# Kernel tuning notes

Hardware: AMD Instinct MI355X
Metric: run time of the kernel (lower is better)

The kernel has to match this reference:

```python
import jax, jax.numpy as jnp
import numpy as np

USER_NUM = 100000
ITEM_NUM = 50000
N_NODES = USER_NUM + ITEM_NUM
NNZ = 4800000
HIDE_DIM = 128
SLOPE = 0.2
EPS = 1e-12  # F.normalize eps


def setup_inputs() -> dict:
    key = jax.random.key(0)
    ks = jax.random.split(key, 9)
    rows = jax.random.randint(ks[0], (NNZ,), 0, N_NODES, dtype=jnp.int32)
    cols = jax.random.randint(ks[1], (NNZ,), 0, N_NODES, dtype=jnp.int32)
    vals = jax.random.uniform(ks[2], (NNZ,), dtype=jnp.float32)
    user_emb = jax.random.normal(ks[3], (USER_NUM, HIDE_DIM), dtype=jnp.float32) * 0.1
    item_emb = jax.random.normal(ks[4], (ITEM_NUM, HIDE_DIM), dtype=jnp.float32) * 0.1
    u_w0 = jax.random.normal(ks[5], (HIDE_DIM, HIDE_DIM), dtype=jnp.float32) * 0.05
    v_w0 = jax.random.normal(ks[6], (HIDE_DIM, HIDE_DIM), dtype=jnp.float32) * 0.05
    u_w1 = jax.random.normal(ks[7], (HIDE_DIM, HIDE_DIM), dtype=jnp.float32) * 0.05
    v_w1 = jax.random.normal(ks[8], (HIDE_DIM, HIDE_DIM), dtype=jnp.float32) * 0.05
    return {"rows": rows, "cols": cols, "vals": vals,
            "user_emb": user_emb, "item_emb": item_emb,
            "u_w0": u_w0, "v_w0": v_w0, "u_w1": u_w1, "v_w1": v_w1}


def _spmm(rows, cols, vals, feat):
    # sparse [N,N] @ dense [N,D] via gather + segment_sum
    gathered = vals[:, None] * feat[cols]            # [nnz, D]
    return jax.ops.segment_sum(gathered, rows, num_segments=N_NODES)


def _gcn_layer(rows, cols, vals, u_feat, i_feat, u_w, v_w):
    feat = jnp.concatenate([u_feat @ u_w, i_feat @ v_w], axis=0)  # [N, D]
    return jax.nn.leaky_relu(_spmm(rows, cols, vals, feat), negative_slope=SLOPE)


def _l2norm(x):
    n = jnp.sqrt(jnp.sum(x * x, axis=1, keepdims=True))
    return x / jnp.maximum(n, EPS)


def reference(rows, cols, vals, user_emb, item_emb, u_w0, v_w0, u_w1, v_w1):
    all_u = [user_emb]
    all_i = [item_emb]
    # layer 0 consumes raw embeddings
    emb = _gcn_layer(rows, cols, vals, user_emb, item_emb, u_w0, v_w0)
    norm = _l2norm(emb)
    all_u.append(norm[:USER_NUM]); all_i.append(norm[USER_NUM:])
    # layer 1 consumes UNNORMALIZED previous layer output (as in the torch code)
    emb = _gcn_layer(rows, cols, vals, emb[:USER_NUM], emb[USER_NUM:], u_w1, v_w1)
    norm = _l2norm(emb)
    all_u.append(norm[:USER_NUM]); all_i.append(norm[USER_NUM:])
    user_embedding = jnp.concatenate(all_u, axis=1)  # [userNum, 3*D]
    item_embedding = jnp.concatenate(all_i, axis=1)  # [itemNum, 3*D]
    return (user_embedding, item_embedding)
```

## Files before the change

### kernel.cpp

```cpp
#include <hip/hip_runtime.h>

#define D 128
#define OUTD 384
#define SLOPE 0.2f
#define BSH 7
#define BROWS 128
#define MAXNB 2048
#define FCAP 4736
#define SPAN 8192
#define SCT 512

typedef __attribute__((ext_vector_type(8))) short bf16x8;
typedef __attribute__((ext_vector_type(4))) float f32x4;

__device__ __forceinline__ unsigned f2bf(float f) {
    unsigned u = __float_as_uint(f);
    return (u + 0x7FFFu + ((u >> 16) & 1u)) >> 16;
}

__device__ __forceinline__ void nt_store_f4(float4 v, float* p) {
    f32x4 t = {v.x, v.y, v.z, v.w};
    __builtin_nontemporal_store(t, (f32x4*)p);
}

__global__ __launch_bounds__(256) void wt_prep(const float* __restrict__ W0,
                                               const float* __restrict__ W1,
                                               const float* __restrict__ W2,
                                               const float* __restrict__ W3,
                                               unsigned short* __restrict__ wt) {
    const float* Ws[4] = {W0, W1, W2, W3};
    const float* W = Ws[blockIdx.x];
    unsigned short* o = wt + (size_t)blockIdx.x * 16384;
    for (int i = threadIdx.x; i < 16384; i += 256) {
        int k = i >> 7, n = i & 127;
        o[(size_t)n * 128 + k] = (unsigned short)f2bf(W[(size_t)k * 128 + n]);
    }
}

#define GR 64
#define APAD 136
__global__ __launch_bounds__(256) void gemm_mfma(const float* __restrict__ in, int pitch,
                                                 const unsigned short* __restrict__ Wt,
                                                 unsigned short* __restrict__ featb,
                                                 const float* __restrict__ rowscale,
                                                 float* __restrict__ rawout,
                                                 int nrows) {
    __shared__ unsigned short sA[GR * APAD];
    __shared__ unsigned short sW[128 * APAD];
    int tid = threadIdx.x;
    int row0 = blockIdx.x * GR;
    int nr = min(GR, nrows - row0);

    for (int i = tid; i < GR * 32; i += 256) {
        int r = i >> 5, c4 = (i & 31) * 4;
        unsigned lo = 0, hi = 0;
        if (r < nr) {
            float4 t = *(const float4*)&in[(size_t)(row0 + r) * pitch + c4];
            if (rawout)
                nt_store_f4(t, &rawout[(size_t)(row0 + r) * OUTD + c4]);
            if (rowscale) {
                float s = rowscale[row0 + r];
                t.x *= s; t.y *= s; t.z *= s; t.w *= s;
            }
            lo = f2bf(t.x) | (f2bf(t.y) << 16);
            hi = f2bf(t.z) | (f2bf(t.w) << 16);
        }
        uint2 pk = {lo, hi};
        *(uint2*)&sA[r * APAD + c4] = pk;
    }
    for (int i = tid; i < 128 * 16; i += 256) {
        int n = i >> 4, k8 = (i & 15) * 8;
        *(uint4*)&sW[n * APAD + k8] = *(const uint4*)&Wt[(size_t)n * 128 + k8];
    }
    __syncthreads();

    int l  = tid & 63;
    int w  = tid >> 6;
    int lr = l & 15;
    int lk = (l >> 4) * 8;

    f32x4 acc[8];
#pragma unroll
    for (int t = 0; t < 8; ++t) acc[t] = (f32x4){0.f, 0.f, 0.f, 0.f};

#pragma unroll
    for (int k0 = 0; k0 < 128; k0 += 32) {
        bf16x8 af = *(const bf16x8*)&sA[(16 * w + lr) * APAD + k0 + lk];
#pragma unroll
        for (int t = 0; t < 8; ++t) {
            bf16x8 bf = *(const bf16x8*)&sW[(t * 16 + lr) * APAD + k0 + lk];
            acc[t] = __builtin_amdgcn_mfma_f32_16x16x32_bf16(af, bf, acc[t], 0, 0, 0);
        }
    }

    int rbase = 16 * w + (l >> 4) * 4;
#pragma unroll
    for (int t = 0; t < 8; ++t) {
#pragma unroll
        for (int q = 0; q < 4; ++q) {
            int r = rbase + q;
            if (r < nr)
                featb[(size_t)(row0 + r) * D + t * 16 + lr] = (unsigned short)f2bf(acc[t][q]);
        }
    }
}


__global__ __launch_bounds__(256) void init_cursors(int* __restrict__ bcursor,
                                                    int NB, int cap) {
    int b = blockIdx.x * 256 + threadIdx.x;
    if (b < NB) bcursor[b * 16] = b * cap;
}

#define EMIT(r, c, v)                                                              \
    {                                                                              \
        int b_ = (r) >> BSH;                                                       \
        int pos_ = atomicAdd(&hist[b_], 1);                                        \
        if ((unsigned)(pos_ - b_ * cap) < (unsigned)cap)                           \
            etmp[pos_] = make_uint2(((unsigned)((r) & (BROWS - 1)) << 18) |        \
                                    (unsigned)(c), __float_as_uint(v));            \
    }

__global__ __launch_bounds__(SCT) void chunk_scatter(const int* __restrict__ rows,
                                                     const int* __restrict__ cols,
                                                     const float* __restrict__ vals,
                                                     int* __restrict__ bcursor,
                                                     uint2* __restrict__ etmp,
                                                     int nnz, int NB, int cap) {
    __shared__ int hist[MAXNB];
    int tid = threadIdx.x;
    int lo  = blockIdx.x * SPAN;
    int hi  = min(lo + SPAN, nnz);
    if (lo >= nnz) return;

    for (int i = tid; i < NB; i += SCT) hist[i] = 0;
    __syncthreads();

    int4 r4[4];
#pragma unroll
    for (int q = 0; q < 4; ++q) {
        int e = lo + (q * SCT + tid) * 4;
        if (e + 3 < hi) {
            r4[q] = *(const int4*)&rows[e];
            atomicAdd(&hist[r4[q].x >> BSH], 1);
            atomicAdd(&hist[r4[q].y >> BSH], 1);
            atomicAdd(&hist[r4[q].z >> BSH], 1);
            atomicAdd(&hist[r4[q].w >> BSH], 1);
        } else {
            int t0 = (e + 0 < hi) ? rows[e + 0] : -1;
            int t1 = (e + 1 < hi) ? rows[e + 1] : -1;
            int t2 = (e + 2 < hi) ? rows[e + 2] : -1;
            int t3 = (e + 3 < hi) ? rows[e + 3] : -1;
            if (t0 >= 0) atomicAdd(&hist[t0 >> BSH], 1);
            if (t1 >= 0) atomicAdd(&hist[t1 >> BSH], 1);
            if (t2 >= 0) atomicAdd(&hist[t2 >> BSH], 1);
            if (t3 >= 0) atomicAdd(&hist[t3 >> BSH], 1);
            r4[q] = make_int4(t0, t1, t2, t3);
        }
    }
    __syncthreads();

    for (int i = tid; i < NB; i += SCT) {
        int c = hist[i];
        hist[i] = c ? atomicAdd(&bcursor[i * 16], c) : 0;
    }
    __syncthreads();

#pragma unroll
    for (int q = 0; q < 4; ++q) {
        int e = lo + (q * SCT + tid) * 4;
        if (e + 3 < hi) {
            int4   c4 = *(const int4*)&cols[e];
            float4 v4 = *(const float4*)&vals[e];
            EMIT(r4[q].x, c4.x, v4.x);
            EMIT(r4[q].y, c4.y, v4.y);
            EMIT(r4[q].z, c4.z, v4.z);
            EMIT(r4[q].w, c4.w, v4.w);
        } else {
            int rr0 = r4[q].x, rr1 = r4[q].y, rr2 = r4[q].z, rr3 = r4[q].w;
            if (rr0 >= 0) { EMIT(rr0, cols[e + 0], vals[e + 0]); }
            if (rr1 >= 0) { EMIT(rr1, cols[e + 1], vals[e + 1]); }
            if (rr2 >= 0) { EMIT(rr2, cols[e + 2], vals[e + 2]); }
            if (rr3 >= 0) { EMIT(rr3, cols[e + 3], vals[e + 3]); }
        }
    }
}

#define FTH 512
__global__ __launch_bounds__(FTH) void bucket_finalize(const int* __restrict__ bcursor,
                                                       uint2* __restrict__ ep,
                                                       int* __restrict__ row_start,
                                                       int* __restrict__ rend,
                                                       int N, int cap) {
    __shared__ uint2 ed[FCAP];
    __shared__ int rcnt[BROWS], rbase[BROWS];
    __shared__ int wsum[2];
    int b   = blockIdx.x;
    int s   = b * cap;
    int len = bcursor[b * 16] - s;
    if (len > cap) len = cap;
    int tid = threadIdx.x;
    if (tid < BROWS) rcnt[tid] = 0;
    __syncthreads();

    for (int i = tid; i < len; i += FTH) {
        uint2 t = ep[s + i];
        ed[i] = t;
        atomicAdd(&rcnt[t.x >> 18], 1);
    }
    __syncthreads();

    int lane = tid & 63, wid = tid >> 6;
    int c = (tid < BROWS) ? rcnt[tid] : 0;
    int incl = c;
#pragma unroll
    for (int off = 1; off < 64; off <<= 1) {
        int t = __shfl_up(incl, off);
        if (lane >= off) incl += t;
    }
    if (tid < BROWS && lane == 63) wsum[wid] = incl;
    __syncthreads();
    if (tid < BROWS) {
        int woff = (wid == 1) ? wsum[0] : 0;
        int excl = woff + incl - c;
        rbase[tid] = s + excl;
        int row = b * BROWS + tid;
        if (row < N) { row_start[row] = s + excl; rend[row] = s + excl + c; }
    }
    __syncthreads();

    for (int i = tid; i < len; i += FTH) {
        uint2 t = ed[i];
        int rl = t.x >> 18;
        int pos = atomicAdd(&rbase[rl], 1);
        ep[pos] = make_uint2(t.x & 0x3FFFFu, t.y);
    }
}

#define ACCQ(vbits, g)                                             \
    {                                                              \
        float v = __uint_as_float(vbits);                          \
        acc0.x += v * __uint_as_float((g).x << 16);                \
        acc0.y += v * __uint_as_float((g).x & 0xFFFF0000u);        \
        acc0.z += v * __uint_as_float((g).y << 16);                \
        acc0.w += v * __uint_as_float((g).y & 0xFFFF0000u);        \
        acc1.x += v * __uint_as_float((g).z << 16);                \
        acc1.y += v * __uint_as_float((g).z & 0xFFFF0000u);        \
        acc1.z += v * __uint_as_float((g).w << 16);                \
        acc1.w += v * __uint_as_float((g).w & 0xFFFF0000u);        \
    }

__global__ __launch_bounds__(256) void spmm_csr4(const uint2* __restrict__ ep,
                                                 const int* __restrict__ rstart,
                                                 const int* __restrict__ rend,
                                                 const unsigned short* __restrict__ featb,
                                                 float* __restrict__ out,
                                                 float* __restrict__ nsave,
                                                 int col_off, int N) {
    int row  = blockIdx.x * 4 + (threadIdx.x >> 6);
    if (row >= N) return;
    int lane = threadIdx.x & 63;
    int j = lane & 15;
    int h = lane >> 4;
    int s = rstart[row], e = rend[row];

    float4 acc0 = {0.f, 0.f, 0.f, 0.f};
    float4 acc1 = {0.f, 0.f, 0.f, 0.f};
    int i = s;
    for (; i + 16 <= e; i += 16) {
        uint2 eA = ep[i + h];
        uint2 eB = ep[i + 4 + h];
        uint2 eC = ep[i + 8 + h];
        uint2 eD = ep[i + 12 + h];
        uint4 gA = *(const uint4*)&featb[(size_t)eA.x * D + j * 8];
        uint4 gB = *(const uint4*)&featb[(size_t)eB.x * D + j * 8];
        uint4 gC = *(const uint4*)&featb[(size_t)eC.x * D + j * 8];
        uint4 gD = *(const uint4*)&featb[(size_t)eD.x * D + j * 8];
        ACCQ(eA.y, gA);
        ACCQ(eB.y, gB);
        ACCQ(eC.y, gC);
        ACCQ(eD.y, gD);
    }
    for (; i + 8 <= e; i += 8) {
        uint2 eA = ep[i + h];
        uint2 eB = ep[i + 4 + h];
        uint4 gA = *(const uint4*)&featb[(size_t)eA.x * D + j * 8];
        uint4 gB = *(const uint4*)&featb[(size_t)eB.x * D + j * 8];
        ACCQ(eA.y, gA);
        ACCQ(eB.y, gB);
    }
    for (; i < e; i += 4) {
        int idx = i + h;
        uint2 ev = make_uint2(0u, 0u);
        if (idx < e) ev = ep[idx];
        uint4 g = *(const uint4*)&featb[(size_t)ev.x * D + j * 8];
        ACCQ(ev.y, g);
    }

#pragma unroll
    for (int m = 16; m <= 32; m <<= 1) {
        acc0.x += __shfl_xor(acc0.x, m);
        acc0.y += __shfl_xor(acc0.y, m);
        acc0.z += __shfl_xor(acc0.z, m);
        acc0.w += __shfl_xor(acc0.w, m);
        acc1.x += __shfl_xor(acc1.x, m);
        acc1.y += __shfl_xor(acc1.y, m);
        acc1.z += __shfl_xor(acc1.z, m);
        acc1.w += __shfl_xor(acc1.w, m);
    }

    acc0.x = (acc0.x > 0.f) ? acc0.x : SLOPE * acc0.x;
    acc0.y = (acc0.y > 0.f) ? acc0.y : SLOPE * acc0.y;
    acc0.z = (acc0.z > 0.f) ? acc0.z : SLOPE * acc0.z;
    acc0.w = (acc0.w > 0.f) ? acc0.w : SLOPE * acc0.w;
    acc1.x = (acc1.x > 0.f) ? acc1.x : SLOPE * acc1.x;
    acc1.y = (acc1.y > 0.f) ? acc1.y : SLOPE * acc1.y;
    acc1.z = (acc1.z > 0.f) ? acc1.z : SLOPE * acc1.z;
    acc1.w = (acc1.w > 0.f) ? acc1.w : SLOPE * acc1.w;

    float ss = acc0.x * acc0.x + acc0.y * acc0.y + acc0.z * acc0.z + acc0.w * acc0.w
             + acc1.x * acc1.x + acc1.y * acc1.y + acc1.z * acc1.z + acc1.w * acc1.w;
#pragma unroll
    for (int m = 8; m >= 1; m >>= 1) ss += __shfl_xor(ss, m);
    float nm = fmaxf(sqrtf(ss), 1e-12f);
    float sc = 1.0f / nm;

    if (nsave && lane == 0) nsave[row] = nm;
    if (h == 0) {
        float* dst = &out[(size_t)row * OUTD + col_off + j * 8];
        float4 o0 = {acc0.x * sc, acc0.y * sc, acc0.z * sc, acc0.w * sc};
        float4 o1 = {acc1.x * sc, acc1.y * sc, acc1.z * sc, acc1.w * sc};
        *(float4*)&dst[0] = o0;
        *(float4*)&dst[4] = o1;
    }
}

extern "C" void kernel_launch(void* const* d_in, const int* in_sizes, int n_in,
                              void* d_out, int out_size, void* d_ws, size_t ws_size,
                              hipStream_t stream) {
    const int*   rows = (const int*)d_in[0];
    const int*   cols = (const int*)d_in[1];
    const float* vals = (const float*)d_in[2];
    const float* ue   = (const float*)d_in[3];
    const float* ie   = (const float*)d_in[4];
    const float* uw0  = (const float*)d_in[5];
    const float* vw0  = (const float*)d_in[6];
    const float* uw1  = (const float*)d_in[7];
    const float* vw1  = (const float*)d_in[8];
    float* out = (float*)d_out;

    int nnz = in_sizes[0];
    int U   = in_sizes[3] / D;
    int I   = in_sizes[4] / D;
    int N   = U + I;
    int NB  = (N + BROWS - 1) >> BSH;

    int avg = nnz / NB;
    int cap = avg + avg / 8 + 64;
    if (cap > FCAP) cap = FCAP;

    char* p = (char*)d_ws;
    unsigned short* featb = (unsigned short*)p;  p += (size_t)N * D * 2;
    uint2* edges          = (uint2*)p;           p += (size_t)NB * cap * 8;
    int* row_start        = (int*)p;             p += (size_t)N * 4;
    int* rend             = (int*)p;             p += (size_t)N * 4;
    float* nsave          = (float*)p;           p += (size_t)N * 4;
    p = (char*)(((size_t)p + 63) & ~(size_t)63);
    int* bcursor          = (int*)p;             p += (size_t)NB * 64;
    unsigned short* wtbuf = (unsigned short*)p;  p += (size_t)4 * 16384 * 2;

    int row_blocks = (N + 3) / 4;
    int gu = (U + GR - 1) / GR;
    int gi = (I + GR - 1) / GR;
    int sc_blocks = (nnz + SPAN - 1) / SPAN;

    wt_prep<<<4, 256, 0, stream>>>(uw0, vw0, uw1, vw1, wtbuf);
    init_cursors<<<(NB + 255) / 256, 256, 0, stream>>>(bcursor, NB, cap);

    chunk_scatter<<<sc_blocks, SCT, 0, stream>>>(rows, cols, vals, bcursor, edges,
                                                 nnz, NB, cap);
    bucket_finalize<<<NB, FTH, 0, stream>>>(bcursor, edges, row_start, rend, N, cap);

    gemm_mfma<<<gu, 256, 0, stream>>>(ue, D, wtbuf, featb, nullptr, out, U);
    gemm_mfma<<<gi, 256, 0, stream>>>(ie, D, wtbuf + 16384, featb + (size_t)U * D,
                                      nullptr, out + (size_t)U * OUTD, I);
    spmm_csr4<<<row_blocks, 256, 0, stream>>>(edges, row_start, rend, featb, out,
                                              nsave, D, N);

    gemm_mfma<<<gu, 256, 0, stream>>>(out + D, OUTD, wtbuf + 2 * 16384, featb,
                                      nsave, nullptr, U);
    gemm_mfma<<<gi, 256, 0, stream>>>(out + (size_t)U * OUTD + D, OUTD, wtbuf + 3 * 16384,
                                      featb + (size_t)U * D, nsave + U, nullptr, I);
    spmm_csr4<<<row_blocks, 256, 0, stream>>>(edges, row_start, rend, featb, out,
                                              nullptr, 2 * D, N);
}
```

Measured before the change: 628.7 us.

## Fuse per-bucket edge sort with first-layer SpMM into one kernel

Merges bucket_finalize and the first spmm_csr4 launch into one kernel. Each 512-thread block sorts its 128-row bucket and then computes SpMM, leaky-ReLU and L2 normalisation for those rows, with each wave handling 16 rows. This removes one launch and lets the just-written sorted edges be read back while likely still cached. In exchange it cuts parallelism to one block per 128 rows, and the large LDS footprint may limit occupancy during the gather phase.

```diff
diff --git a/kernel.cpp b/kernel.cpp
--- a/kernel.cpp
+++ b/kernel.cpp
@@ -104,7 +104,6 @@
         }
     }
 }
-
 
 __global__ __launch_bounds__(256) void init_cursors(int* __restrict__ bcursor,
                                                     int NB, int cap) {
@@ -186,57 +185,6 @@
     }
 }
 
-#define FTH 512
-__global__ __launch_bounds__(FTH) void bucket_finalize(const int* __restrict__ bcursor,
-                                                       uint2* __restrict__ ep,
-                                                       int* __restrict__ row_start,
-                                                       int* __restrict__ rend,
-                                                       int N, int cap) {
-    __shared__ uint2 ed[FCAP];
-    __shared__ int rcnt[BROWS], rbase[BROWS];
-    __shared__ int wsum[2];
-    int b   = blockIdx.x;
-    int s   = b * cap;
-    int len = bcursor[b * 16] - s;
-    if (len > cap) len = cap;
-    int tid = threadIdx.x;
-    if (tid < BROWS) rcnt[tid] = 0;
-    __syncthreads();
-
-    for (int i = tid; i < len; i += FTH) {
-        uint2 t = ep[s + i];
-        ed[i] = t;
-        atomicAdd(&rcnt[t.x >> 18], 1);
-    }
-    __syncthreads();
-
-    int lane = tid & 63, wid = tid >> 6;
-    int c = (tid < BROWS) ? rcnt[tid] : 0;
-    int incl = c;
-#pragma unroll
-    for (int off = 1; off < 64; off <<= 1) {
-        int t = __shfl_up(incl, off);
-        if (lane >= off) incl += t;
-    }
-    if (tid < BROWS && lane == 63) wsum[wid] = incl;
-    __syncthreads();
-    if (tid < BROWS) {
-        int woff = (wid == 1) ? wsum[0] : 0;
-        int excl = woff + incl - c;
-        rbase[tid] = s + excl;
-        int row = b * BROWS + tid;
-        if (row < N) { row_start[row] = s + excl; rend[row] = s + excl + c; }
-    }
-    __syncthreads();
-
-    for (int i = tid; i < len; i += FTH) {
-        uint2 t = ed[i];
-        int rl = t.x >> 18;
-        int pos = atomicAdd(&rbase[rl], 1);
-        ep[pos] = make_uint2(t.x & 0x3FFFFu, t.y);
-    }
-}
-
 #define ACCQ(vbits, g)                                             \
     {                                                              \
         float v = __uint_as_float(vbits);                          \
@@ -250,12 +198,146 @@
         acc1.w += v * __uint_as_float((g).w & 0xFFFF0000u);        \
     }
 
+#define FTH 512
+__global__ __launch_bounds__(FTH) void spmm_sort_fused(const int* __restrict__ bcursor,
+                                                       uint2* __restrict__ ep,
+                                                       int* __restrict__ row_start,
+                                                       int* __restrict__ rend,
+                                                       const unsigned short* __restrict__ featb,
+                                                       float* __restrict__ out,
+                                                       float* __restrict__ nsave,
+                                                       int col_off, int N, int cap) {
+    __shared__ uint2 ed[FCAP];
+    __shared__ int rcnt[BROWS], rbase[BROWS], rsLds[BROWS];
+    __shared__ int wsum[2];
+    int b   = blockIdx.x;
+    int s   = b * cap;
+    int len = bcursor[b * 16] - s;
+    if (len > cap) len = cap;
+    int tid = threadIdx.x;
+    if (tid < BROWS) rcnt[tid] = 0;
+    __syncthreads();
+
+    for (int i = tid; i < len; i += FTH) {
+        uint2 t = ep[s + i];
+        ed[i] = t;
+        atomicAdd(&rcnt[t.x >> 18], 1);
+    }
+    __syncthreads();
+
+    int lane = tid & 63, wid = tid >> 6;
+    int c = (tid < BROWS) ? rcnt[tid] : 0;
+    int incl = c;
+#pragma unroll
+    for (int off = 1; off < 64; off <<= 1) {
+        int t = __shfl_up(incl, off);
+        if (lane >= off) incl += t;
+    }
+    if (tid < BROWS && lane == 63) wsum[wid] = incl;
+    __syncthreads();
+    if (tid < BROWS) {
+        int woff = (wid == 1) ? wsum[0] : 0;
+        int excl = woff + incl - c;
+        rbase[tid] = s + excl;
+        rsLds[tid] = s + excl;
+        int row = b * BROWS + tid;
+        if (row < N) { row_start[row] = s + excl; rend[row] = s + excl + c; }
+    }
+    __syncthreads();
+
+    for (int i = tid; i < len; i += FTH) {
+        uint2 t = ed[i];
+        int pos = atomicAdd(&rbase[t.x >> 18], 1);
+        ep[pos] = make_uint2(t.x & 0x3FFFFu, t.y);
+    }
+    __syncthreads();
+
+    int j = lane & 15;
+    int h = lane >> 4;
+    for (int rr = 0; rr < 16; ++rr) {
+        int rloc = wid * 16 + rr;
+        int row  = b * BROWS + rloc;
+        if (row >= N) break;
+        int sE = rsLds[rloc];
+        int eE = sE + rcnt[rloc];
+
+        float4 acc0 = {0.f, 0.f, 0.f, 0.f};
+        float4 acc1 = {0.f, 0.f, 0.f, 0.f};
+        int i = sE;
+        for (; i + 16 <= eE; i += 16) {
+            uint2 eA = ep[i + h];
+            uint2 eB = ep[i + 4 + h];
+            uint2 eC = ep[i + 8 + h];
+            uint2 eD = ep[i + 12 + h];
+            uint4 gA = *(const uint4*)&featb[(size_t)eA.x * D + j * 8];
+            uint4 gB = *(const uint4*)&featb[(size_t)eB.x * D + j * 8];
+            uint4 gC = *(const uint4*)&featb[(size_t)eC.x * D + j * 8];
+            uint4 gD = *(const uint4*)&featb[(size_t)eD.x * D + j * 8];
+            ACCQ(eA.y, gA);
+            ACCQ(eB.y, gB);
+            ACCQ(eC.y, gC);
+            ACCQ(eD.y, gD);
+        }
+        for (; i + 8 <= eE; i += 8) {
+            uint2 eA = ep[i + h];
+            uint2 eB = ep[i + 4 + h];
+            uint4 gA = *(const uint4*)&featb[(size_t)eA.x * D + j * 8];
+            uint4 gB = *(const uint4*)&featb[(size_t)eB.x * D + j * 8];
+            ACCQ(eA.y, gA);
+            ACCQ(eB.y, gB);
+        }
+        for (; i < eE; i += 4) {
+            int idx = i + h;
+            uint2 ev = make_uint2(0u, 0u);
+            if (idx < eE) ev = ep[idx];
+            uint4 g = *(const uint4*)&featb[(size_t)ev.x * D + j * 8];
+            ACCQ(ev.y, g);
+        }
+
+#pragma unroll
+        for (int m = 16; m <= 32; m <<= 1) {
+            acc0.x += __shfl_xor(acc0.x, m);
+            acc0.y += __shfl_xor(acc0.y, m);
+            acc0.z += __shfl_xor(acc0.z, m);
+            acc0.w += __shfl_xor(acc0.w, m);
+            acc1.x += __shfl_xor(acc1.x, m);
+            acc1.y += __shfl_xor(acc1.y, m);
+            acc1.z += __shfl_xor(acc1.z, m);
+            acc1.w += __shfl_xor(acc1.w, m);
+        }
+
+        acc0.x = (acc0.x > 0.f) ? acc0.x : SLOPE * acc0.x;
+        acc0.y = (acc0.y > 0.f) ? acc0.y : SLOPE * acc0.y;
+        acc0.z = (acc0.z > 0.f) ? acc0.z : SLOPE * acc0.z;
+        acc0.w = (acc0.w > 0.f) ? acc0.w : SLOPE * acc0.w;
+        acc1.x = (acc1.x > 0.f) ? acc1.x : SLOPE * acc1.x;
+        acc1.y = (acc1.y > 0.f) ? acc1.y : SLOPE * acc1.y;
+        acc1.z = (acc1.z > 0.f) ? acc1.z : SLOPE * acc1.z;
+        acc1.w = (acc1.w > 0.f) ? acc1.w : SLOPE * acc1.w;
+
+        float ss = acc0.x * acc0.x + acc0.y * acc0.y + acc0.z * acc0.z + acc0.w * acc0.w
+                 + acc1.x * acc1.x + acc1.y * acc1.y + acc1.z * acc1.z + acc1.w * acc1.w;
+#pragma unroll
+        for (int m = 8; m >= 1; m >>= 1) ss += __shfl_xor(ss, m);
+        float nm = fmaxf(sqrtf(ss), 1e-12f);
+        float sc = 1.0f / nm;
+
+        if (lane == 0) nsave[row] = nm;
+        if (h == 0) {
+            float* dst = &out[(size_t)row * OUTD + col_off + j * 8];
+            float4 o0 = {acc0.x * sc, acc0.y * sc, acc0.z * sc, acc0.w * sc};
+            float4 o1 = {acc1.x * sc, acc1.y * sc, acc1.z * sc, acc1.w * sc};
+            *(float4*)&dst[0] = o0;
+            *(float4*)&dst[4] = o1;
+        }
+    }
+}
+
 __global__ __launch_bounds__(256) void spmm_csr4(const uint2* __restrict__ ep,
                                                  const int* __restrict__ rstart,
                                                  const int* __restrict__ rend,
                                                  const unsigned short* __restrict__ featb,
                                                  float* __restrict__ out,
-                                                 float* __restrict__ nsave,
                                                  int col_off, int N) {
     int row  = blockIdx.x * 4 + (threadIdx.x >> 6);
     if (row >= N) return;
@@ -322,10 +404,8 @@
              + acc1.x * acc1.x + acc1.y * acc1.y + acc1.z * acc1.z + acc1.w * acc1.w;
 #pragma unroll
     for (int m = 8; m >= 1; m >>= 1) ss += __shfl_xor(ss, m);
-    float nm = fmaxf(sqrtf(ss), 1e-12f);
-    float sc = 1.0f / nm;
-
-    if (nsave && lane == 0) nsave[row] = nm;
+    float sc = 1.0f / fmaxf(sqrtf(ss), 1e-12f);
+
     if (h == 0) {
         float* dst = &out[(size_t)row * OUTD + col_off + j * 8];
         float4 o0 = {acc0.x * sc, acc0.y * sc, acc0.z * sc, acc0.w * sc};
@@ -379,18 +459,18 @@
 
     chunk_scatter<<<sc_blocks, SCT, 0, stream>>>(rows, cols, vals, bcursor, edges,
                                                  nnz, NB, cap);
-    bucket_finalize<<<NB, FTH, 0, stream>>>(bcursor, edges, row_start, rend, N, cap);
 
     gemm_mfma<<<gu, 256, 0, stream>>>(ue, D, wtbuf, featb, nullptr, out, U);
     gemm_mfma<<<gi, 256, 0, stream>>>(ie, D, wtbuf + 16384, featb + (size_t)U * D,
                                       nullptr, out + (size_t)U * OUTD, I);
-    spmm_csr4<<<row_blocks, 256, 0, stream>>>(edges, row_start, rend, featb, out,
-                                              nsave, D, N);
+
+    spmm_sort_fused<<<NB, FTH, 0, stream>>>(bcursor, edges, row_start, rend, featb,
+                                            out, nsave, D, N, cap);
 
     gemm_mfma<<<gu, 256, 0, stream>>>(out + D, OUTD, wtbuf + 2 * 16384, featb,
                                       nsave, nullptr, U);
     gemm_mfma<<<gi, 256, 0, stream>>>(out + (size_t)U * OUTD + D, OUTD, wtbuf + 3 * 16384,
                                       featb + (size_t)U * D, nsave + U, nullptr, I);
     spmm_csr4<<<row_blocks, 256, 0, stream>>>(edges, row_start, rend, featb, out,
-                                              nullptr, 2 * D, N);
-}
+                                              2 * D, N);
+}
```

Result: slower. 648.4 us (+3.1%).

## Replace global-atomic bucket scatter with per-segment local sort plus offset matrix

Applied to the files above, without the earlier changes.

The COO-to-CSR build no longer uses global atomic cursors per bucket. Each segment now sorts its edges by bucket locally into a temporary buffer and writes a per-segment offset matrix. The finalize kernel gathers every segment's slice for its bucket into LDS and then writes row-sorted edges to a separate buffer. This removes contended global atomics and the init kernel. In exchange it adds a second full edge buffer aliased with featb, and finalize copies each segment slice with a serial per-thread loop.

```diff
diff --git a/kernel.cpp b/kernel.cpp
--- a/kernel.cpp
+++ b/kernel.cpp
@@ -9,6 +9,8 @@
 #define FCAP 4736
 #define SPAN 8192
 #define SCT 512
+#define FTH 512
+#define NSMAX 1024
 
 typedef __attribute__((ext_vector_type(8))) short bf16x8;
 typedef __attribute__((ext_vector_type(4))) float f32x4;
@@ -105,31 +107,17 @@
     }
 }
 
-
-__global__ __launch_bounds__(256) void init_cursors(int* __restrict__ bcursor,
-                                                    int NB, int cap) {
-    int b = blockIdx.x * 256 + threadIdx.x;
-    if (b < NB) bcursor[b * 16] = b * cap;
-}
-
-#define EMIT(r, c, v)                                                              \
-    {                                                                              \
-        int b_ = (r) >> BSH;                                                       \
-        int pos_ = atomicAdd(&hist[b_], 1);                                        \
-        if ((unsigned)(pos_ - b_ * cap) < (unsigned)cap)                           \
-            etmp[pos_] = make_uint2(((unsigned)((r) & (BROWS - 1)) << 18) |        \
-                                    (unsigned)(c), __float_as_uint(v));            \
-    }
-
-__global__ __launch_bounds__(SCT) void chunk_scatter(const int* __restrict__ rows,
-                                                     const int* __restrict__ cols,
-                                                     const float* __restrict__ vals,
-                                                     int* __restrict__ bcursor,
-                                                     uint2* __restrict__ etmp,
-                                                     int nnz, int NB, int cap) {
+__global__ __launch_bounds__(SCT) void seg_scatter(const int* __restrict__ rows,
+                                                   const int* __restrict__ cols,
+                                                   const float* __restrict__ vals,
+                                                   uint2* __restrict__ etmp,
+                                                   int* __restrict__ offmat,
+                                                   int nnz, int NB) {
     __shared__ int hist[MAXNB];
+    __shared__ int wsum[8];
     int tid = threadIdx.x;
-    int lo  = blockIdx.x * SPAN;
+    int sgm = blockIdx.x;
+    int lo  = sgm * SPAN;
     int hi  = min(lo + SPAN, nnz);
     if (lo >= nnz) return;
 
@@ -160,80 +148,165 @@
     }
     __syncthreads();
 
-    for (int i = tid; i < NB; i += SCT) {
-        int c = hist[i];
-        hist[i] = c ? atomicAdd(&bcursor[i * 16], c) : 0;
-    }
-    __syncthreads();
-
+    int per = (NB + SCT - 1) / SCT;
+    int base = tid * per;
+    int lv[4];
+    int lsum = 0;
+#pragma unroll
+    for (int k = 0; k < 4; ++k) {
+        int idx = base + k;
+        int v = (k < per && idx < NB) ? hist[idx] : 0;
+        lv[k] = v; lsum += v;
+    }
+    int lane = tid & 63, wid = tid >> 6;
+    int incl = lsum;
+#pragma unroll
+    for (int off = 1; off < 64; off <<= 1) {
+        int t = __shfl_up(incl, off);
+        if (lane >= off) incl += t;
+    }
+    if (lane == 63) wsum[wid] = incl;
+    __syncthreads();
+    int woff = 0;
+    for (int w = 0; w < wid; ++w) woff += wsum[w];
+    int run = woff + incl - lsum;
+    __syncthreads();
+    int rowbase = sgm * (NB + 1);
+#pragma unroll
+    for (int k = 0; k < 4; ++k) {
+        int idx = base + k;
+        if (k < per && idx < NB) {
+            int c = lv[k];
+            hist[idx] = run;
+            offmat[rowbase + idx] = run;
+            run += c;
+        }
+    }
+    if (NB - 1 >= base && NB - 1 < base + per)
+        offmat[rowbase + NB] = run;
+    __syncthreads();
+
+#define SEMIT(r, c, v)                                                             \
+    {                                                                              \
+        int pos_ = atomicAdd(&hist[(r) >> BSH], 1);                                \
+        etmp[lo + pos_] = make_uint2(((unsigned)((r) & (BROWS - 1)) << 18) |       \
+                                     (unsigned)(c), __float_as_uint(v));           \
+    }
 #pragma unroll
     for (int q = 0; q < 4; ++q) {
         int e = lo + (q * SCT + tid) * 4;
         if (e + 3 < hi) {
             int4   c4 = *(const int4*)&cols[e];
             float4 v4 = *(const float4*)&vals[e];
-            EMIT(r4[q].x, c4.x, v4.x);
-            EMIT(r4[q].y, c4.y, v4.y);
-            EMIT(r4[q].z, c4.z, v4.z);
-            EMIT(r4[q].w, c4.w, v4.w);
+            SEMIT(r4[q].x, c4.x, v4.x);
+            SEMIT(r4[q].y, c4.y, v4.y);
+            SEMIT(r4[q].z, c4.z, v4.z);
+            SEMIT(r4[q].w, c4.w, v4.w);
         } else {
             int rr0 = r4[q].x, rr1 = r4[q].y, rr2 = r4[q].z, rr3 = r4[q].w;
-            if (rr0 >= 0) { EMIT(rr0, cols[e + 0], vals[e + 0]); }
-            if (rr1 >= 0) { EMIT(rr1, cols[e + 1], vals[e + 1]); }
-            if (rr2 >= 0) { EMIT(rr2, cols[e + 2], vals[e + 2]); }
-            if (rr3 >= 0) { EMIT(rr3, cols[e + 3], vals[e + 3]); }
-        }
-    }
-}
-
-#define FTH 512
-__global__ __launch_bounds__(FTH) void bucket_finalize(const int* __restrict__ bcursor,
-                                                       uint2* __restrict__ ep,
-                                                       int* __restrict__ row_start,
-                                                       int* __restrict__ rend,
-                                                       int N, int cap) {
+            if (rr0 >= 0) { SEMIT(rr0, cols[e + 0], vals[e + 0]); }
+            if (rr1 >= 0) { SEMIT(rr1, cols[e + 1], vals[e + 1]); }
+            if (rr2 >= 0) { SEMIT(rr2, cols[e + 2], vals[e + 2]); }
+            if (rr3 >= 0) { SEMIT(rr3, cols[e + 3], vals[e + 3]); }
+        }
+    }
+}
+
+__global__ __launch_bounds__(FTH) void seg_finalize(const uint2* __restrict__ etmp,
+                                                    const int* __restrict__ offmat,
+                                                    uint2* __restrict__ esort,
+                                                    int* __restrict__ row_start,
+                                                    int* __restrict__ rend,
+                                                    int N, int NB, int NS, int cap) {
     __shared__ uint2 ed[FCAP];
+    __shared__ int srcoff[NSMAX], slen[NSMAX], dstoff[NSMAX];
     __shared__ int rcnt[BROWS], rbase[BROWS];
-    __shared__ int wsum[2];
+    __shared__ int wsum[8];
+    __shared__ int tot;
     int b   = blockIdx.x;
-    int s   = b * cap;
-    int len = bcursor[b * 16] - s;
-    if (len > cap) len = cap;
     int tid = threadIdx.x;
+    int lane = tid & 63, wid = tid >> 6;
     if (tid < BROWS) rcnt[tid] = 0;
-    __syncthreads();
-
-    for (int i = tid; i < len; i += FTH) {
-        uint2 t = ep[s + i];
-        ed[i] = t;
-        atomicAdd(&rcnt[t.x >> 18], 1);
-    }
-    __syncthreads();
-
-    int lane = tid & 63, wid = tid >> 6;
-    int c = (tid < BROWS) ? rcnt[tid] : 0;
-    int incl = c;
+
+    int per = (NS + FTH - 1) / FTH;
+    int base = tid * per;
+    int lo0[2], ll[2];
+    int lsum = 0;
+#pragma unroll
+    for (int k = 0; k < 2; ++k) {
+        int s = base + k;
+        int o0 = 0, l = 0;
+        if (k < per && s < NS) {
+            int rb = s * (NB + 1) + b;
+            o0 = offmat[rb];
+            l  = offmat[rb + 1] - o0;
+        }
+        lo0[k] = o0; ll[k] = l; lsum += l;
+    }
+    int incl = lsum;
 #pragma unroll
     for (int off = 1; off < 64; off <<= 1) {
         int t = __shfl_up(incl, off);
         if (lane >= off) incl += t;
     }
-    if (tid < BROWS && lane == 63) wsum[wid] = incl;
+    if (lane == 63) wsum[wid] = incl;
+    __syncthreads();
+    int woff = 0;
+    for (int w = 0; w < wid; ++w) woff += wsum[w];
+    int run = woff + incl - lsum;
+#pragma unroll
+    for (int k = 0; k < 2; ++k) {
+        int s = base + k;
+        if (k < per && s < NS) {
+            srcoff[s] = lo0[k];
+            slen[s]   = ll[k];
+            dstoff[s] = run;
+            run += ll[k];
+        }
+    }
+    if (NS - 1 >= base && NS - 1 < base + per) tot = min(run, cap);
+    __syncthreads();
+
+#pragma unroll
+    for (int k = 0; k < 2; ++k) {
+        int s = base + k;
+        if (k < per && s < NS) {
+            int src = s * SPAN + srcoff[s];
+            int dst = dstoff[s];
+            int l   = slen[s];
+            if (dst + l > cap) l = max(0, cap - dst);
+            for (int i2 = 0; i2 < l; ++i2) {
+                uint2 t = etmp[src + i2];
+                ed[dst + i2] = t;
+                atomicAdd(&rcnt[t.x >> 18], 1);
+            }
+        }
+    }
+    __syncthreads();
+
+    int c = (tid < BROWS) ? rcnt[tid] : 0;
+    int incl2 = c;
+#pragma unroll
+    for (int off = 1; off < 64; off <<= 1) {
+        int t = __shfl_up(incl2, off);
+        if (lane >= off) incl2 += t;
+    }
+    if (tid < BROWS && lane == 63) wsum[wid] = incl2;
     __syncthreads();
     if (tid < BROWS) {
-        int woff = (wid == 1) ? wsum[0] : 0;
-        int excl = woff + incl - c;
-        rbase[tid] = s + excl;
+        int woff2 = (wid == 1) ? wsum[0] : 0;
+        int excl = woff2 + incl2 - c;
+        rbase[tid] = b * cap + excl;
         int row = b * BROWS + tid;
-        if (row < N) { row_start[row] = s + excl; rend[row] = s + excl + c; }
-    }
-    __syncthreads();
-
-    for (int i = tid; i < len; i += FTH) {
-        uint2 t = ed[i];
-        int rl = t.x >> 18;
-        int pos = atomicAdd(&rbase[rl], 1);
-        ep[pos] = make_uint2(t.x & 0x3FFFFu, t.y);
+        if (row < N) { row_start[row] = b * cap + excl; rend[row] = b * cap + excl + c; }
+    }
+    __syncthreads();
+
+    int tl = tot;
+    for (int i2 = tid; i2 < tl; i2 += FTH) {
+        uint2 t = ed[i2];
+        int pos = atomicAdd(&rbase[t.x >> 18], 1);
+        esort[pos] = make_uint2(t.x & 0x3FFFFu, t.y);
     }
 }
 
@@ -354,43 +427,46 @@
     int I   = in_sizes[4] / D;
     int N   = U + I;
     int NB  = (N + BROWS - 1) >> BSH;
+    int NS  = (nnz + SPAN - 1) / SPAN;
 
     int avg = nnz / NB;
     int cap = avg + avg / 8 + 64;
     if (cap > FCAP) cap = FCAP;
 
     char* p = (char*)d_ws;
-    unsigned short* featb = (unsigned short*)p;  p += (size_t)N * D * 2;
-    uint2* edges          = (uint2*)p;           p += (size_t)NB * cap * 8;
+    size_t unionSz = (size_t)N * D * 2;
+    if ((size_t)nnz * 8 > unionSz) unionSz = (size_t)nnz * 8;
+    unsigned short* featb = (unsigned short*)p;
+    uint2*          etmp  = (uint2*)p;           p += unionSz;
+    uint2* esort          = (uint2*)p;           p += (size_t)NB * cap * 8;
     int* row_start        = (int*)p;             p += (size_t)N * 4;
     int* rend             = (int*)p;             p += (size_t)N * 4;
     float* nsave          = (float*)p;           p += (size_t)N * 4;
     p = (char*)(((size_t)p + 63) & ~(size_t)63);
-    int* bcursor          = (int*)p;             p += (size_t)NB * 64;
+    int* offmat           = (int*)p;             p += (size_t)NS * (NB + 1) * 4;
+    p = (char*)(((size_t)p + 63) & ~(size_t)63);
     unsigned short* wtbuf = (unsigned short*)p;  p += (size_t)4 * 16384 * 2;
 
     int row_blocks = (N + 3) / 4;
     int gu = (U + GR - 1) / GR;
     int gi = (I + GR - 1) / GR;
-    int sc_blocks = (nnz + SPAN - 1) / SPAN;
 
     wt_prep<<<4, 256, 0, stream>>>(uw0, vw0, uw1, vw1, wtbuf);
-    init_cursors<<<(NB + 255) / 256, 256, 0, stream>>>(bcursor, NB, cap);
-
-    chunk_scatter<<<sc_blocks, SCT, 0, stream>>>(rows, cols, vals, bcursor, edges,
-                                                 nnz, NB, cap);
-    bucket_finalize<<<NB, FTH, 0, stream>>>(bcursor, edges, row_start, rend, N, cap);
+
+    seg_scatter<<<NS, SCT, 0, stream>>>(rows, cols, vals, etmp, offmat, nnz, NB);
+    seg_finalize<<<NB, FTH, 0, stream>>>(etmp, offmat, esort, row_start, rend,
+                                         N, NB, NS, cap);
 
     gemm_mfma<<<gu, 256, 0, stream>>>(ue, D, wtbuf, featb, nullptr, out, U);
     gemm_mfma<<<gi, 256, 0, stream>>>(ie, D, wtbuf + 16384, featb + (size_t)U * D,
                                       nullptr, out + (size_t)U * OUTD, I);
-    spmm_csr4<<<row_blocks, 256, 0, stream>>>(edges, row_start, rend, featb, out,
+    spmm_csr4<<<row_blocks, 256, 0, stream>>>(esort, row_start, rend, featb, out,
                                               nsave, D, N);
 
     gemm_mfma<<<gu, 256, 0, stream>>>(out + D, OUTD, wtbuf + 2 * 16384, featb,
                                       nsave, nullptr, U);
     gemm_mfma<<<gi, 256, 0, stream>>>(out + (size_t)U * OUTD + D, OUTD, wtbuf + 3 * 16384,
                                       featb + (size_t)U * D, nsave + U, nullptr, I);
-    spmm_csr4<<<row_blocks, 256, 0, stream>>>(edges, row_start, rend, featb, out,
+    spmm_csr4<<<row_blocks, 256, 0, stream>>>(esort, row_start, rend, featb, out,
                                               nullptr, 2 * D, N);
 }
```

Result: faster. 583.3 us (-7.2%).
